# Kernel tuning notes

Measured on AMD Instinct MI355X. Metric: run time of the kernel, lower is better.

## Reference

```python
import jax, jax.numpy as jnp
import numpy as np

H = 2048       # hidden_size
NH = 16        # num_attention_heads
NKV = 4        # num_key_value_heads
HD = H // NH   # head_dim = 128
INTER = 8192   # intermediate_size
L = 2048       # packed sequence length
EPS = 1e-6


def rmsnorm(x, w, eps=EPS):
    var = jnp.mean(x * x, axis=-1, keepdims=True)
    return x * jax.lax.rsqrt(var + eps) * w


def setup_inputs() -> dict:
    key = jax.random.key(0)
    ks = jax.random.split(key, 9)
    s = 0.02
    return {
        "hidden_states": jax.random.normal(ks[0], (1, L, H), jnp.float32),
        "cu_seqlens_q": jnp.array([0, 512, 1280, 2048], jnp.int32),
        "ln1_w": jnp.ones((H,), jnp.float32),
        "ln2_w": jnp.ones((H,), jnp.float32),
        "q_w": jax.random.normal(ks[1], (NH * HD, H), jnp.float32) * s,
        "k_w": jax.random.normal(ks[2], (NKV * HD, H), jnp.float32) * s,
        "v_w": jax.random.normal(ks[3], (NKV * HD, H), jnp.float32) * s,
        "o_w": jax.random.normal(ks[4], (H, NH * HD), jnp.float32) * s,
        "gate_w": jax.random.normal(ks[5], (INTER, H), jnp.float32) * s,
        "up_w": jax.random.normal(ks[6], (INTER, H), jnp.float32) * s,
        "down_w": jax.random.normal(ks[7], (H, INTER), jnp.float32) * s,
    }


def _segment_mask(cu, q_len):
    # segment id of each position: repeat_interleave of arange over lengths
    pos = jnp.arange(q_len)
    seg = jnp.searchsorted(cu[1:], pos, side="right")  # [L]
    mask = seg[:, None] == seg[None, :]
    mask = mask & (pos[None, :] <= pos[:, None])  # causal, q_len == k_len
    return mask  # [L, L] bool


def _forward(hidden_states, cu_seqlens_q, ln1_w, ln2_w, q_w, k_w, v_w, o_w,
             gate_w, up_w, down_w):
    b, q_len, _ = hidden_states.shape
    residual = hidden_states
    normed = rmsnorm(hidden_states, ln1_w)

    # project_kv
    key_states = (normed @ k_w.T).reshape(b, q_len, NKV, HD)
    value_states = (normed @ v_w.T).reshape(b, q_len, NKV, HD)

    q = (normed @ q_w.T).reshape(b, q_len, NH, HD)
    rep = NH // NKV
    k = jnp.repeat(key_states, rep, axis=2)   # repeat_interleave over heads
    v = jnp.repeat(value_states, rep, axis=2)

    scores = jnp.einsum("bqhd,bkhd->bhqk", q, k) / np.sqrt(HD)
    mask = _segment_mask(cu_seqlens_q, q_len)
    scores = jnp.where(mask[None, None, :, :], scores,
                       jnp.finfo(scores.dtype).min)
    probs = jax.nn.softmax(scores.astype(jnp.float32), axis=-1).astype(q.dtype)
    attn = jnp.einsum("bhqk,bkhd->bqhd", probs, v).reshape(b, q_len, NH * HD)
    mixed = attn @ o_w.T

    hidden = residual + mixed
    residual = hidden
    normed2 = rmsnorm(hidden, ln2_w)
    mlp = (jax.nn.silu(normed2 @ gate_w.T) * (normed2 @ up_w.T)) @ down_w.T
    hidden = residual + mlp
    return hidden, key_states, value_states


def reference(hidden_states, cu_seqlens_q, ln1_w, ln2_w, q_w, k_w, v_w, o_w,
              gate_w, up_w, down_w):
    return _forward(hidden_states, cu_seqlens_q, ln1_w, ln2_w, q_w, k_w, v_w,
                    o_w, gate_w, up_w, down_w)
```

## Files before the change

kernel.cpp:

```cpp
#include <hip/hip_runtime.h>
#include <stdint.h>

typedef __bf16 bf16;
typedef __bf16 bf16x8 __attribute__((ext_vector_type(8)));
typedef float f32x4 __attribute__((ext_vector_type(4)));

#define L_SEQ 2048
#define H_DIM 2048
#define KV_DIM 512
#define QKV_LD 3072
#define INTER_DIM 8192

__device__ __forceinline__ void load_lds16(const void* g, void* l) {
  __builtin_amdgcn_global_load_lds(
      (const __attribute__((address_space(1))) void*)g,
      (__attribute__((address_space(3))) void*)l, 16, 0, 0);
}

__global__ __launch_bounds__(256)
void cvt_bf16(const float* __restrict__ s, bf16* __restrict__ d) {
  const size_t i = ((size_t)blockIdx.x * 256 + threadIdx.x) * 8;
  float4 a = *(const float4*)(s + i);
  float4 b = *(const float4*)(s + i + 4);
  bf16x8 o;
  o[0] = (bf16)a.x; o[1] = (bf16)a.y; o[2] = (bf16)a.z; o[3] = (bf16)a.w;
  o[4] = (bf16)b.x; o[5] = (bf16)b.y; o[6] = (bf16)b.z; o[7] = (bf16)b.w;
  *(bf16x8*)(d + i) = o;
}

__global__ __launch_bounds__(256)
void rmsnorm_bf16(const float* __restrict__ x, const float* __restrict__ w,
                  bf16* __restrict__ out) {
  const int row = blockIdx.x;
  const int t = threadIdx.x;
  const float* xr = x + (size_t)row * H_DIM + t * 8;
  float4 a = *(const float4*)xr;
  float4 b = *(const float4*)(xr + 4);
  float ss = a.x * a.x + a.y * a.y + a.z * a.z + a.w * a.w +
             b.x * b.x + b.y * b.y + b.z * b.z + b.w * b.w;
#pragma unroll
  for (int off = 1; off < 64; off <<= 1) ss += __shfl_xor(ss, off, 64);
  __shared__ float red[4];
  if ((t & 63) == 0) red[t >> 6] = ss;
  __syncthreads();
  ss = red[0] + red[1] + red[2] + red[3];
  const float rs = rsqrtf(ss * (1.0f / H_DIM) + 1e-6f);
  float4 w1 = *(const float4*)(w + t * 8);
  float4 w2 = *(const float4*)(w + t * 8 + 4);
  bf16x8 o;
  o[0] = (bf16)(a.x * rs * w1.x);
  o[1] = (bf16)(a.y * rs * w1.y);
  o[2] = (bf16)(a.z * rs * w1.z);
  o[3] = (bf16)(a.w * rs * w1.w);
  o[4] = (bf16)(b.x * rs * w2.x);
  o[5] = (bf16)(b.y * rs * w2.y);
  o[6] = (bf16)(b.z * rs * w2.z);
  o[7] = (bf16)(b.w * rs * w2.w);
  *(bf16x8*)(out + (size_t)row * H_DIM + t * 8) = o;
}

enum { M_PART = 0, M_QKV = 1 };

template <int MODE>
__global__ __launch_bounds__(256, 2)
void gemm_bt(const bf16* __restrict__ A, int lda,
             const bf16* __restrict__ B, int ldb, int kpb,
             bf16* __restrict__ outb, int ldob,
             float* __restrict__ outf, int ldof, size_t zstride,
             float* __restrict__ outk, float* __restrict__ outv) {
  __shared__ bf16 sA[128 * 32];
  __shared__ bf16 sB[128 * 32];
  const int t = threadIdx.x;
  const int lane = t & 63;
  const int l15 = lane & 15, l4 = lane >> 4;
  const int wm = ((t >> 6) >> 1) * 64;
  const int wn = ((t >> 6) & 1) * 64;
  const int m0 = blockIdx.y * 128;
  const int n0 = blockIdx.x * 128;
  const int kbeg = blockIdx.z * kpb;
  const int kend = kbeg + kpb;

  const f32x4 zero = {0.f, 0.f, 0.f, 0.f};
  f32x4 acc[4][4];
#pragma unroll
  for (int i = 0; i < 4; ++i)
#pragma unroll
    for (int j = 0; j < 4; ++j) acc[i][j] = zero;

  for (int k0 = kbeg; k0 < kend; k0 += 32) {
#pragma unroll
    for (int i = 0; i < 2; ++i) {
      const int flat = i * 4096 + t * 16;
      const int r = flat >> 6, cb = (flat & 63) >> 1;
      load_lds16(A + (size_t)(m0 + r) * lda + k0 + cb, (char*)sA + flat);
      load_lds16(B + (size_t)(n0 + r) * ldb + k0 + cb, (char*)sB + flat);
    }
    __syncthreads();

    bf16x8 af[4], bfr[4];
#pragma unroll
    for (int mi = 0; mi < 4; ++mi)
      af[mi] = *(const bf16x8*)(&sA[(wm + mi * 16 + l15) * 32 + l4 * 8]);
#pragma unroll
    for (int ni = 0; ni < 4; ++ni)
      bfr[ni] = *(const bf16x8*)(&sB[(wn + ni * 16 + l15) * 32 + l4 * 8]);
#pragma unroll
    for (int mi = 0; mi < 4; ++mi)
#pragma unroll
      for (int ni = 0; ni < 4; ++ni)
        acc[mi][ni] = __builtin_amdgcn_mfma_f32_16x16x32_bf16(
            af[mi], bfr[ni], acc[mi][ni], 0, 0, 0);
    __syncthreads();
  }

#pragma unroll
  for (int mi = 0; mi < 4; ++mi) {
#pragma unroll
    for (int ni = 0; ni < 4; ++ni) {
      const int row0 = m0 + wm + mi * 16 + l4 * 4;
      const int col = n0 + wn + ni * 16 + l15;
#pragma unroll
      for (int r = 0; r < 4; ++r) {
        const float c = acc[mi][ni][r];
        const size_t m = (size_t)(row0 + r);
        if (MODE == M_PART) {
          outf[zstride * blockIdx.z + m * ldof + col] = c;
        } else {
          outb[m * QKV_LD + col] = (bf16)c;
          if (col >= 2560)      outv[m * KV_DIM + (col - 2560)] = c;
          else if (col >= 2048) outk[m * KV_DIM + (col - 2048)] = c;
        }
      }
    }
  }
}

__global__ __launch_bounds__(256, 2)
void gemm_glu(const bf16* __restrict__ A, const bf16* __restrict__ Bg,
              const bf16* __restrict__ Bu, bf16* __restrict__ out) {
  __shared__ bf16 sA[128 * 32];
  __shared__ bf16 sG[128 * 32];
  __shared__ bf16 sU[128 * 32];
  const int t = threadIdx.x;
  const int lane = t & 63;
  const int l15 = lane & 15, l4 = lane >> 4;
  const int wm = ((t >> 6) >> 1) * 64;
  const int wn = ((t >> 6) & 1) * 64;
  const int m0 = blockIdx.y * 128;
  const int n0 = blockIdx.x * 128;

  const f32x4 zero = {0.f, 0.f, 0.f, 0.f};
  f32x4 ag[4][4], au[4][4];
#pragma unroll
  for (int i = 0; i < 4; ++i)
#pragma unroll
    for (int j = 0; j < 4; ++j) { ag[i][j] = zero; au[i][j] = zero; }

  for (int k0 = 0; k0 < H_DIM; k0 += 32) {
#pragma unroll
    for (int i = 0; i < 2; ++i) {
      const int flat = i * 4096 + t * 16;
      const int r = flat >> 6, cb = (flat & 63) >> 1;
      load_lds16(A + (size_t)(m0 + r) * H_DIM + k0 + cb, (char*)sA + flat);
      load_lds16(Bg + (size_t)(n0 + r) * H_DIM + k0 + cb, (char*)sG + flat);
      load_lds16(Bu + (size_t)(n0 + r) * H_DIM + k0 + cb, (char*)sU + flat);
    }
    __syncthreads();

    bf16x8 af[4], bg[4], bu[4];
#pragma unroll
    for (int mi = 0; mi < 4; ++mi)
      af[mi] = *(const bf16x8*)(&sA[(wm + mi * 16 + l15) * 32 + l4 * 8]);
#pragma unroll
    for (int ni = 0; ni < 4; ++ni) {
      bg[ni] = *(const bf16x8*)(&sG[(wn + ni * 16 + l15) * 32 + l4 * 8]);
      bu[ni] = *(const bf16x8*)(&sU[(wn + ni * 16 + l15) * 32 + l4 * 8]);
    }
#pragma unroll
    for (int mi = 0; mi < 4; ++mi)
#pragma unroll
      for (int ni = 0; ni < 4; ++ni) {
        ag[mi][ni] = __builtin_amdgcn_mfma_f32_16x16x32_bf16(
            af[mi], bg[ni], ag[mi][ni], 0, 0, 0);
        au[mi][ni] = __builtin_amdgcn_mfma_f32_16x16x32_bf16(
            af[mi], bu[ni], au[mi][ni], 0, 0, 0);
      }
    __syncthreads();
  }

#pragma unroll
  for (int mi = 0; mi < 4; ++mi) {
#pragma unroll
    for (int ni = 0; ni < 4; ++ni) {
      const int row0 = m0 + wm + mi * 16 + l4 * 4;
      const int col = n0 + wn + ni * 16 + l15;
#pragma unroll
      for (int r = 0; r < 4; ++r) {
        const float g = ag[mi][ni][r];
        const float u = au[mi][ni][r];
        const float s = g / (1.f + __expf(-g));
        out[(size_t)(row0 + r) * INTER_DIM + col] = (bf16)(s * u);
      }
    }
  }
}

__global__ __launch_bounds__(256)
void reduce_add2(const float* __restrict__ p0, const float* __restrict__ p1,
                 const float* __restrict__ res, float* __restrict__ out) {
  const size_t i = ((size_t)blockIdx.x * 256 + threadIdx.x) * 4;
  float4 a = *(const float4*)(p0 + i);
  float4 b = *(const float4*)(p1 + i);
  float4 c = *(const float4*)(res + i);
  float4 o;
  o.x = a.x + b.x + c.x;
  o.y = a.y + b.y + c.y;
  o.z = a.z + b.z + c.z;
  o.w = a.w + b.w + c.w;
  *(float4*)(out + i) = o;
}

__global__ __launch_bounds__(256, 2)
void attn_fwd(const bf16* __restrict__ qkv, const int* __restrict__ cu,
              bf16* __restrict__ out) {
  const int h = blockIdx.y;
  const int q0 = blockIdx.x * 64;
  const int kvh = h >> 2;
  const int t = threadIdx.x;
  const int lane = t & 63;
  const int w = t >> 6;
  const int l15 = lane & 15, l4 = lane >> 4;

  __shared__ bf16 sK[64 * 136];
  __shared__ bf16 sV[64 * 136];
  __shared__ bf16 sP[4][16 * 64];

  const int c1 = cu[1], c2 = cu[2];
  const int seg0 = (q0 >= c2) ? c2 : ((q0 >= c1) ? c1 : 0);

  const int qrow = q0 + w * 16 + l15;
  bf16x8 qf[4];
#pragma unroll
  for (int kc = 0; kc < 4; ++kc) {
    bf16x8 v = *(const bf16x8*)(qkv + (size_t)qrow * QKV_LD + h * 128 +
                                kc * 32 + l4 * 8);
#pragma unroll
    for (int j = 0; j < 8; ++j)
      v[j] = (bf16)((float)v[j] * 0.08838834764831845f);
    qf[kc] = v;
  }

  const f32x4 zero = {0.f, 0.f, 0.f, 0.f};
  f32x4 oacc[8];
#pragma unroll
  for (int i = 0; i < 8; ++i) oacc[i] = zero;
  float mi[4] = {-1e30f, -1e30f, -1e30f, -1e30f};
  float li[4] = {0.f, 0.f, 0.f, 0.f};

  for (int k0 = seg0; k0 <= q0; k0 += 64) {
#pragma unroll
    for (int it = 0; it < 4; ++it) {
      const int flat = it * 4096 + t * 16;
      const int r = flat >> 8, db = flat & 255;
      const char* krow =
          (const char*)(qkv + (size_t)(k0 + r) * QKV_LD + 2048 + kvh * 128);
      const char* vrow =
          (const char*)(qkv + (size_t)(k0 + r) * QKV_LD + 2560 + kvh * 128);
      *(bf16x8*)((char*)sK + r * 272 + db) = *(const bf16x8*)(krow + db);
      *(bf16x8*)((char*)sV + r * 272 + db) = *(const bf16x8*)(vrow + db);
    }
    __syncthreads();

    f32x4 sacc[4];
#pragma unroll
    for (int kg = 0; kg < 4; ++kg) {
      f32x4 a = zero;
#pragma unroll
      for (int kc = 0; kc < 4; ++kc) {
        bf16x8 kf = *(const bf16x8*)((const char*)sK +
                                     (kg * 16 + l15) * 272 + kc * 64 + l4 * 16);
        a = __builtin_amdgcn_mfma_f32_16x16x32_bf16(qf[kc], kf, a, 0, 0, 0);
      }
      sacc[kg] = a;
    }

    if (k0 == q0) {
#pragma unroll
      for (int kg = 0; kg < 4; ++kg) {
        const int kk = kg * 16 + l15;
#pragma unroll
        for (int r = 0; r < 4; ++r) {
          const int qq = w * 16 + l4 * 4 + r;
          if (kk > qq) sacc[kg][r] = -1e30f;
        }
      }
    }

    float mx[4], al[4], rs[4];
#pragma unroll
    for (int r = 0; r < 4; ++r)
      mx[r] = fmaxf(fmaxf(sacc[0][r], sacc[1][r]),
                    fmaxf(sacc[2][r], sacc[3][r]));
#pragma unroll
    for (int off = 1; off < 16; off <<= 1)
#pragma unroll
      for (int r = 0; r < 4; ++r)
        mx[r] = fmaxf(mx[r], __shfl_xor(mx[r], off, 64));
#pragma unroll
    for (int r = 0; r < 4; ++r) {
      const float mn = fmaxf(mi[r], mx[r]);
      al[r] = __expf(mi[r] - mn);
      mi[r] = mn;
      rs[r] = 0.f;
    }
#pragma unroll
    for (int kg = 0; kg < 4; ++kg)
#pragma unroll
      for (int r = 0; r < 4; ++r) {
        const float p = __expf(sacc[kg][r] - mi[r]);
        sacc[kg][r] = p;
        rs[r] += p;
      }
#pragma unroll
    for (int off = 1; off < 16; off <<= 1)
#pragma unroll
      for (int r = 0; r < 4; ++r) rs[r] += __shfl_xor(rs[r], off, 64);
#pragma unroll
    for (int r = 0; r < 4; ++r) li[r] = li[r] * al[r] + rs[r];
#pragma unroll
    for (int dn = 0; dn < 8; ++dn)
#pragma unroll
      for (int r = 0; r < 4; ++r) oacc[dn][r] *= al[r];

#pragma unroll
    for (int kg = 0; kg < 4; ++kg)
#pragma unroll
      for (int r = 0; r < 4; ++r)
        sP[w][(l4 * 4 + r) * 64 + kg * 16 + l15] = (bf16)sacc[kg][r];
    __syncthreads();

    bf16x8 pf[2];
#pragma unroll
    for (int kc2 = 0; kc2 < 2; ++kc2)
      pf[kc2] = *(const bf16x8*)(&sP[w][l15 * 64 + kc2 * 32 + l4 * 8]);
#pragma unroll
    for (int dn = 0; dn < 8; ++dn)
#pragma unroll
      for (int kc2 = 0; kc2 < 2; ++kc2) {
        bf16x8 vf;
#pragma unroll
        for (int j = 0; j < 8; ++j)
          vf[j] = sV[(kc2 * 32 + l4 * 8 + j) * 136 + dn * 16 + l15];
        oacc[dn] =
            __builtin_amdgcn_mfma_f32_16x16x32_bf16(pf[kc2], vf, oacc[dn], 0, 0, 0);
      }
    __syncthreads();
  }

#pragma unroll
  for (int dn = 0; dn < 8; ++dn)
#pragma unroll
    for (int r = 0; r < 4; ++r) {
      const size_t m = (size_t)(q0 + w * 16 + l4 * 4 + r);
      out[m * H_DIM + h * 128 + dn * 16 + l15] = (bf16)(oacc[dn][r] / li[r]);
    }
}

extern "C" void kernel_launch(void* const* d_in, const int* in_sizes, int n_in,
                              void* d_out, int out_size, void* d_ws,
                              size_t ws_size, hipStream_t stream) {
  (void)in_sizes; (void)n_in; (void)out_size; (void)ws_size;
  const float* hs     = (const float*)d_in[0];
  const int*   cu     = (const int*)d_in[1];
  const float* ln1    = (const float*)d_in[2];
  const float* ln2    = (const float*)d_in[3];
  const float* q_w    = (const float*)d_in[4];
  const float* k_w    = (const float*)d_in[5];
  const float* v_w    = (const float*)d_in[6];
  const float* o_w    = (const float*)d_in[7];
  const float* gate_w = (const float*)d_in[8];
  const float* up_w   = (const float*)d_in[9];
  const float* down_w = (const float*)d_in[10];

  float* out_hidden = (float*)d_out;
  float* out_k = out_hidden + (size_t)L_SEQ * H_DIM;
  float* out_v = out_k + (size_t)L_SEQ * KV_DIM;

  char* ws = (char*)d_ws;
  bf16* WB = (bf16*)ws;
  const size_t wq_off = 0;
  const size_t wk_off = 4194304;
  const size_t wv_off = 5242880;
  const size_t wo_off = 6291456;
  const size_t wg_off = 10485760;
  const size_t wu_off = 27262976;
  const size_t wd_off = 44040192;

  bf16*  normed1 = (bf16*)(ws + ((size_t)116 << 20));
  bf16*  qkv     = (bf16*)(ws + ((size_t)124 << 20));
  bf16*  attnb   = (bf16*)(ws + ((size_t)136 << 20));
  bf16*  normed2 = (bf16*)(ws + ((size_t)144 << 20));
  bf16*  interb  = (bf16*)(ws + ((size_t)152 << 20));
  float* opart   = (float*)(ws + ((size_t)152 << 20));
  float* dpart   = (float*)(ws + ((size_t)116 << 20));

  dim3 blk(256);

  cvt_bf16<<<2048, blk, 0, stream>>>(q_w,    WB + wq_off);
  cvt_bf16<<< 512, blk, 0, stream>>>(k_w,    WB + wk_off);
  cvt_bf16<<< 512, blk, 0, stream>>>(v_w,    WB + wv_off);
  cvt_bf16<<<2048, blk, 0, stream>>>(o_w,    WB + wo_off);
  cvt_bf16<<<8192, blk, 0, stream>>>(gate_w, WB + wg_off);
  cvt_bf16<<<8192, blk, 0, stream>>>(up_w,   WB + wu_off);
  cvt_bf16<<<8192, blk, 0, stream>>>(down_w, WB + wd_off);

  rmsnorm_bf16<<<L_SEQ, blk, 0, stream>>>(hs, ln1, normed1);

  gemm_bt<M_QKV><<<dim3(24, 16, 1), blk, 0, stream>>>(
      normed1, H_DIM, WB + wq_off, H_DIM, H_DIM, qkv, QKV_LD, nullptr, 0, 0,
      out_k, out_v);

  attn_fwd<<<dim3(32, 16), blk, 0, stream>>>(qkv, cu, attnb);

  gemm_bt<M_PART><<<dim3(16, 16, 2), blk, 0, stream>>>(
      attnb, H_DIM, WB + wo_off, H_DIM, 1024, nullptr, 0, opart, H_DIM,
      (size_t)L_SEQ * H_DIM, nullptr, nullptr);
  reduce_add2<<<4096, blk, 0, stream>>>(opart, opart + (size_t)L_SEQ * H_DIM,
                                        hs, out_hidden);

  rmsnorm_bf16<<<L_SEQ, blk, 0, stream>>>(out_hidden, ln2, normed2);

  gemm_glu<<<dim3(64, 16), blk, 0, stream>>>(normed2, WB + wg_off, WB + wu_off,
                                             interb);

  gemm_bt<M_PART><<<dim3(16, 16, 2), blk, 0, stream>>>(
      interb, INTER_DIM, WB + wd_off, INTER_DIM, 4096, nullptr, 0, dpart,
      H_DIM, (size_t)L_SEQ * H_DIM, nullptr, nullptr);
  reduce_add2<<<4096, blk, 0, stream>>>(dpart, dpart + (size_t)L_SEQ * H_DIM,
                                        out_hidden, out_hidden);
}
```

Baseline: 705.1 us.

## Fuse weight conversions and add+rmsnorm, transpose V in LDS, split-K 4 down proj

Merges the seven weight-conversion launches into one kernel and fuses the residual reduce with the second RMSNorm into a single kernel. In attention, V is stored transposed in shared memory so each MFMA B-fragment is one vector load instead of eight scalar reads, and the barrier after writing P is dropped because each wave's P buffer is private. The down projection now splits K four ways, which needs a four-way reduce and a relocated partial buffer. The risks are LDS bank conflicts from the scalar transposed stores and the extra partial-sum traffic of the deeper split-K.

```diff
diff --git a/kernel.cpp b/kernel.cpp
--- a/kernel.cpp
+++ b/kernel.cpp
@@ -18,14 +18,28 @@
 }
 
 __global__ __launch_bounds__(256)
-void cvt_bf16(const float* __restrict__ s, bf16* __restrict__ d) {
-  const size_t i = ((size_t)blockIdx.x * 256 + threadIdx.x) * 8;
+void cvt_all(const float* __restrict__ q, const float* __restrict__ k,
+             const float* __restrict__ v, const float* __restrict__ o,
+             const float* __restrict__ g, const float* __restrict__ u,
+             const float* __restrict__ dn, bf16* __restrict__ WB) {
+  const int b = blockIdx.x;
+  const float* s;
+  size_t doff;
+  int lb;
+  if (b < 2048)       { s = q;  doff = 0;        lb = b; }
+  else if (b < 2560)  { s = k;  doff = 4194304;  lb = b - 2048; }
+  else if (b < 3072)  { s = v;  doff = 5242880;  lb = b - 2560; }
+  else if (b < 5120)  { s = o;  doff = 6291456;  lb = b - 3072; }
+  else if (b < 13312) { s = g;  doff = 10485760; lb = b - 5120; }
+  else if (b < 21504) { s = u;  doff = 27262976; lb = b - 13312; }
+  else                { s = dn; doff = 44040192; lb = b - 21504; }
+  const size_t i = (size_t)lb * 2048 + threadIdx.x * 8;
   float4 a = *(const float4*)(s + i);
-  float4 b = *(const float4*)(s + i + 4);
-  bf16x8 o;
-  o[0] = (bf16)a.x; o[1] = (bf16)a.y; o[2] = (bf16)a.z; o[3] = (bf16)a.w;
-  o[4] = (bf16)b.x; o[5] = (bf16)b.y; o[6] = (bf16)b.z; o[7] = (bf16)b.w;
-  *(bf16x8*)(d + i) = o;
+  float4 c = *(const float4*)(s + i + 4);
+  bf16x8 ov;
+  ov[0] = (bf16)a.x; ov[1] = (bf16)a.y; ov[2] = (bf16)a.z; ov[3] = (bf16)a.w;
+  ov[4] = (bf16)c.x; ov[5] = (bf16)c.y; ov[6] = (bf16)c.z; ov[7] = (bf16)c.w;
+  *(bf16x8*)(WB + doff + i) = ov;
 }
 
 __global__ __launch_bounds__(256)
@@ -59,13 +73,73 @@
   *(bf16x8*)(out + (size_t)row * H_DIM + t * 8) = o;
 }
 
+__global__ __launch_bounds__(256)
+void add_rmsnorm(const float* __restrict__ p0, const float* __restrict__ p1,
+                 const float* __restrict__ res, const float* __restrict__ w,
+                 float* __restrict__ hidden, bf16* __restrict__ normed) {
+  const int row = blockIdx.x;
+  const int t = threadIdx.x;
+  const size_t base = (size_t)row * H_DIM + t * 8;
+  float4 a0 = *(const float4*)(p0 + base);
+  float4 a1 = *(const float4*)(p0 + base + 4);
+  float4 b0 = *(const float4*)(p1 + base);
+  float4 b1 = *(const float4*)(p1 + base + 4);
+  float4 c0 = *(const float4*)(res + base);
+  float4 c1 = *(const float4*)(res + base + 4);
+  float4 h0, h1;
+  h0.x = a0.x + b0.x + c0.x; h0.y = a0.y + b0.y + c0.y;
+  h0.z = a0.z + b0.z + c0.z; h0.w = a0.w + b0.w + c0.w;
+  h1.x = a1.x + b1.x + c1.x; h1.y = a1.y + b1.y + c1.y;
+  h1.z = a1.z + b1.z + c1.z; h1.w = a1.w + b1.w + c1.w;
+  *(float4*)(hidden + base) = h0;
+  *(float4*)(hidden + base + 4) = h1;
+  float ss = h0.x * h0.x + h0.y * h0.y + h0.z * h0.z + h0.w * h0.w +
+             h1.x * h1.x + h1.y * h1.y + h1.z * h1.z + h1.w * h1.w;
+#pragma unroll
+  for (int off = 1; off < 64; off <<= 1) ss += __shfl_xor(ss, off, 64);
+  __shared__ float red[4];
+  if ((t & 63) == 0) red[t >> 6] = ss;
+  __syncthreads();
+  ss = red[0] + red[1] + red[2] + red[3];
+  const float rs = rsqrtf(ss * (1.0f / H_DIM) + 1e-6f);
+  float4 w1 = *(const float4*)(w + t * 8);
+  float4 w2 = *(const float4*)(w + t * 8 + 4);
+  bf16x8 o;
+  o[0] = (bf16)(h0.x * rs * w1.x);
+  o[1] = (bf16)(h0.y * rs * w1.y);
+  o[2] = (bf16)(h0.z * rs * w1.z);
+  o[3] = (bf16)(h0.w * rs * w1.w);
+  o[4] = (bf16)(h1.x * rs * w2.x);
+  o[5] = (bf16)(h1.y * rs * w2.y);
+  o[6] = (bf16)(h1.z * rs * w2.z);
+  o[7] = (bf16)(h1.w * rs * w2.w);
+  *(bf16x8*)(normed + (size_t)row * H_DIM + t * 8) = o;
+}
+
+__global__ __launch_bounds__(256)
+void reduce_add4(const float* __restrict__ p, size_t zs,
+                 const float* __restrict__ res, float* __restrict__ out) {
+  const size_t i = ((size_t)blockIdx.x * 256 + threadIdx.x) * 4;
+  float4 a = *(const float4*)(p + i);
+  float4 b = *(const float4*)(p + zs + i);
+  float4 c = *(const float4*)(p + 2 * zs + i);
+  float4 d = *(const float4*)(p + 3 * zs + i);
+  float4 r = *(const float4*)(res + i);
+  float4 o;
+  o.x = a.x + b.x + c.x + d.x + r.x;
+  o.y = a.y + b.y + c.y + d.y + r.y;
+  o.z = a.z + b.z + c.z + d.z + r.z;
+  o.w = a.w + b.w + c.w + d.w + r.w;
+  *(float4*)(out + i) = o;
+}
+
 enum { M_PART = 0, M_QKV = 1 };
 
 template <int MODE>
 __global__ __launch_bounds__(256, 2)
 void gemm_bt(const bf16* __restrict__ A, int lda,
              const bf16* __restrict__ B, int ldb, int kpb,
-             bf16* __restrict__ outb, int ldob,
+             bf16* __restrict__ outb,
              float* __restrict__ outf, int ldof, size_t zstride,
              float* __restrict__ outk, float* __restrict__ outv) {
   __shared__ bf16 sA[128 * 32];
@@ -205,21 +279,6 @@
   }
 }
 
-__global__ __launch_bounds__(256)
-void reduce_add2(const float* __restrict__ p0, const float* __restrict__ p1,
-                 const float* __restrict__ res, float* __restrict__ out) {
-  const size_t i = ((size_t)blockIdx.x * 256 + threadIdx.x) * 4;
-  float4 a = *(const float4*)(p0 + i);
-  float4 b = *(const float4*)(p1 + i);
-  float4 c = *(const float4*)(res + i);
-  float4 o;
-  o.x = a.x + b.x + c.x;
-  o.y = a.y + b.y + c.y;
-  o.z = a.z + b.z + c.z;
-  o.w = a.w + b.w + c.w;
-  *(float4*)(out + i) = o;
-}
-
 __global__ __launch_bounds__(256, 2)
 void attn_fwd(const bf16* __restrict__ qkv, const int* __restrict__ cu,
               bf16* __restrict__ out) {
@@ -232,7 +291,7 @@
   const int l15 = lane & 15, l4 = lane >> 4;
 
   __shared__ bf16 sK[64 * 136];
-  __shared__ bf16 sV[64 * 136];
+  __shared__ bf16 sVt[128 * 72];
   __shared__ bf16 sP[4][16 * 64];
 
   const int c1 = cu[1], c2 = cu[2];
@@ -262,12 +321,15 @@
     for (int it = 0; it < 4; ++it) {
       const int flat = it * 4096 + t * 16;
       const int r = flat >> 8, db = flat & 255;
-      const char* krow =
-          (const char*)(qkv + (size_t)(k0 + r) * QKV_LD + 2048 + kvh * 128);
-      const char* vrow =
-          (const char*)(qkv + (size_t)(k0 + r) * QKV_LD + 2560 + kvh * 128);
-      *(bf16x8*)((char*)sK + r * 272 + db) = *(const bf16x8*)(krow + db);
-      *(bf16x8*)((char*)sV + r * 272 + db) = *(const bf16x8*)(vrow + db);
+      *(bf16x8*)((char*)sK + r * 272 + db) = *(const bf16x8*)(
+          (const char*)(qkv + (size_t)(k0 + r) * QKV_LD + 2048 + kvh * 128) +
+          db);
+      const int chunk = it * 256 + t;
+      const int vr = chunk & 63, dc = chunk >> 6;
+      bf16x8 vv = *(const bf16x8*)(qkv + (size_t)(k0 + vr) * QKV_LD + 2560 +
+                                   kvh * 128 + dc * 8);
+#pragma unroll
+      for (int j = 0; j < 8; ++j) sVt[(dc * 8 + j) * 72 + vr] = vv[j];
     }
     __syncthreads();
 
@@ -277,8 +339,8 @@
       f32x4 a = zero;
 #pragma unroll
       for (int kc = 0; kc < 4; ++kc) {
-        bf16x8 kf = *(const bf16x8*)((const char*)sK +
-                                     (kg * 16 + l15) * 272 + kc * 64 + l4 * 16);
+        bf16x8 kf = *(const bf16x8*)((const char*)sK + (kg * 16 + l15) * 272 +
+                                     kc * 64 + l4 * 16);
         a = __builtin_amdgcn_mfma_f32_16x16x32_bf16(qf[kc], kf, a, 0, 0, 0);
       }
       sacc[kg] = a;
@@ -337,7 +399,6 @@
 #pragma unroll
       for (int r = 0; r < 4; ++r)
         sP[w][(l4 * 4 + r) * 64 + kg * 16 + l15] = (bf16)sacc[kg][r];
-    __syncthreads();
 
     bf16x8 pf[2];
 #pragma unroll
@@ -347,12 +408,10 @@
     for (int dn = 0; dn < 8; ++dn)
 #pragma unroll
       for (int kc2 = 0; kc2 < 2; ++kc2) {
-        bf16x8 vf;
-#pragma unroll
-        for (int j = 0; j < 8; ++j)
-          vf[j] = sV[(kc2 * 32 + l4 * 8 + j) * 136 + dn * 16 + l15];
-        oacc[dn] =
-            __builtin_amdgcn_mfma_f32_16x16x32_bf16(pf[kc2], vf, oacc[dn], 0, 0, 0);
+        bf16x8 vf = *(const bf16x8*)(&sVt[(dn * 16 + l15) * 72 + kc2 * 32 +
+                                          l4 * 8]);
+        oacc[dn] = __builtin_amdgcn_mfma_f32_16x16x32_bf16(pf[kc2], vf,
+                                                           oacc[dn], 0, 0, 0);
       }
     __syncthreads();
   }
@@ -389,8 +448,6 @@
   char* ws = (char*)d_ws;
   bf16* WB = (bf16*)ws;
   const size_t wq_off = 0;
-  const size_t wk_off = 4194304;
-  const size_t wv_off = 5242880;
   const size_t wo_off = 6291456;
   const size_t wg_off = 10485760;
   const size_t wu_off = 27262976;
@@ -402,40 +459,35 @@
   bf16*  normed2 = (bf16*)(ws + ((size_t)144 << 20));
   bf16*  interb  = (bf16*)(ws + ((size_t)152 << 20));
   float* opart   = (float*)(ws + ((size_t)152 << 20));
-  float* dpart   = (float*)(ws + ((size_t)116 << 20));
+  float* dpart   = (float*)(ws + ((size_t)20 << 20));
 
   dim3 blk(256);
 
-  cvt_bf16<<<2048, blk, 0, stream>>>(q_w,    WB + wq_off);
-  cvt_bf16<<< 512, blk, 0, stream>>>(k_w,    WB + wk_off);
-  cvt_bf16<<< 512, blk, 0, stream>>>(v_w,    WB + wv_off);
-  cvt_bf16<<<2048, blk, 0, stream>>>(o_w,    WB + wo_off);
-  cvt_bf16<<<8192, blk, 0, stream>>>(gate_w, WB + wg_off);
-  cvt_bf16<<<8192, blk, 0, stream>>>(up_w,   WB + wu_off);
-  cvt_bf16<<<8192, blk, 0, stream>>>(down_w, WB + wd_off);
+  cvt_all<<<29696, blk, 0, stream>>>(q_w, k_w, v_w, o_w, gate_w, up_w, down_w,
+                                     WB);
 
   rmsnorm_bf16<<<L_SEQ, blk, 0, stream>>>(hs, ln1, normed1);
 
   gemm_bt<M_QKV><<<dim3(24, 16, 1), blk, 0, stream>>>(
-      normed1, H_DIM, WB + wq_off, H_DIM, H_DIM, qkv, QKV_LD, nullptr, 0, 0,
-      out_k, out_v);
+      normed1, H_DIM, WB + wq_off, H_DIM, H_DIM, qkv, nullptr, 0, 0, out_k,
+      out_v);
 
   attn_fwd<<<dim3(32, 16), blk, 0, stream>>>(qkv, cu, attnb);
 
   gemm_bt<M_PART><<<dim3(16, 16, 2), blk, 0, stream>>>(
-      attnb, H_DIM, WB + wo_off, H_DIM, 1024, nullptr, 0, opart, H_DIM,
+      attnb, H_DIM, WB + wo_off, H_DIM, 1024, nullptr, opart, H_DIM,
       (size_t)L_SEQ * H_DIM, nullptr, nullptr);
-  reduce_add2<<<4096, blk, 0, stream>>>(opart, opart + (size_t)L_SEQ * H_DIM,
-                                        hs, out_hidden);
-
-  rmsnorm_bf16<<<L_SEQ, blk, 0, stream>>>(out_hidden, ln2, normed2);
+
+  add_rmsnorm<<<L_SEQ, blk, 0, stream>>>(opart, opart + (size_t)L_SEQ * H_DIM,
+                                         hs, ln2, out_hidden, normed2);
 
   gemm_glu<<<dim3(64, 16), blk, 0, stream>>>(normed2, WB + wg_off, WB + wu_off,
                                              interb);
 
-  gemm_bt<M_PART><<<dim3(16, 16, 2), blk, 0, stream>>>(
-      interb, INTER_DIM, WB + wd_off, INTER_DIM, 4096, nullptr, 0, dpart,
-      H_DIM, (size_t)L_SEQ * H_DIM, nullptr, nullptr);
-  reduce_add2<<<4096, blk, 0, stream>>>(dpart, dpart + (size_t)L_SEQ * H_DIM,
+  gemm_bt<M_PART><<<dim3(16, 16, 4), blk, 0, stream>>>(
+      interb, INTER_DIM, WB + wd_off, INTER_DIM, 2048, nullptr, dpart, H_DIM,
+      (size_t)L_SEQ * H_DIM, nullptr, nullptr);
+
+  reduce_add4<<<4096, blk, 0, stream>>>(dpart, (size_t)L_SEQ * H_DIM,
                                         out_hidden, out_hidden);
 }
```

After: 665.0 us. 1.06x faster.
